# Kernel tuning notes

Measured on AMD Instinct MI355X. Metric: run time of the kernel, lower is better.

Reference implementation:

```python
import jax, jax.numpy as jnp
import numpy as np

B, N, C = 16, 1024, 768
H, HD = 9, 64  # num_active_heads, head_dim


def setup_inputs() -> dict:
    key = jax.random.key(0)
    ks = jax.random.split(key, 5)
    x = jax.random.normal(ks[0], (B, N, C), dtype=jnp.float32)
    qkv_w = jax.random.normal(ks[1], (3 * H * HD, C), dtype=jnp.float32) * (1.0 / np.sqrt(C))
    qkv_b = jax.random.normal(ks[2], (3 * H * HD,), dtype=jnp.float32) * 0.02
    proj_w = jax.random.normal(ks[3], (C, H * HD), dtype=jnp.float32) * (1.0 / np.sqrt(H * HD))
    proj_b = jax.random.normal(ks[4], (C,), dtype=jnp.float32) * 0.02
    return {"x": x, "qkv_w": qkv_w, "qkv_b": qkv_b, "proj_w": proj_w, "proj_b": proj_b}


def reference(x, qkv_w, qkv_b, proj_w, proj_b):
    b, n, c = x.shape
    # qkv projection: [B,N,3*H*HD] -> [3,B,H,N,HD]
    qkv = (x @ qkv_w.T + qkv_b).reshape(b, n, 3, H, HD).transpose(2, 0, 3, 1, 4)
    q, k, v = qkv[0], qkv[1], qkv[2]
    scale = HD ** -0.5
    attn = jnp.einsum('bhqd,bhkd->bhqk', q, k) * scale  # [B,H,N,N]
    attn = jax.nn.softmax(attn, axis=-1)
    out = jnp.einsum('bhqk,bhkd->bhqd', attn, v)  # [B,H,N,HD]
    out = out.transpose(0, 2, 1, 3).reshape(b, n, H * HD)
    return out @ proj_w.T + proj_b
```

## Files before the change

kernel.cpp:

```cpp
#include <hip/hip_runtime.h>


typedef _Float16 f16x8 __attribute__((ext_vector_type(8)));
typedef _Float16 f16x4 __attribute__((ext_vector_type(4)));
typedef __fp16   h16x2 __attribute__((ext_vector_type(2)));
typedef float    f32x4 __attribute__((ext_vector_type(4)));

#define MFMA16(a, b, c) __builtin_amdgcn_mfma_f32_16x16x32_f16(a, b, c, 0, 0, 0)

__device__ __forceinline__ void gld16(const _Float16* g, _Float16* l) {
  __builtin_amdgcn_global_load_lds((const __attribute__((address_space(1))) void*)g,
                                   (__attribute__((address_space(3))) void*)l, 16, 0, 0);
}

__global__ __launch_bounds__(256) void cvt_swz(const float* __restrict__ src,
                                               _Float16* __restrict__ dst,
                                               int rows_src, int cpr, int total) {
  const int g = blockIdx.x * 256 + threadIdx.x;
  if (g >= total) return;
  const int row = g / cpr;
  const int c = g - row * cpr;
  const int L = cpr * 8;
  const int pos = (c & ~7) | ((c ^ row) & 7);
  union { f16x8 v; h16x2 h[4]; } u;
  if (row < rows_src) {
    const float4 a = *(const float4*)(src + row * L + c * 8);
    const float4 b = *(const float4*)(src + row * L + c * 8 + 4);
    u.h[0] = __builtin_amdgcn_cvt_pkrtz(a.x, a.y);
    u.h[1] = __builtin_amdgcn_cvt_pkrtz(a.z, a.w);
    u.h[2] = __builtin_amdgcn_cvt_pkrtz(b.x, b.y);
    u.h[3] = __builtin_amdgcn_cvt_pkrtz(b.z, b.w);
  } else {
    u.v = (f16x8){};
  }
  *(f16x8*)(dst + row * L + pos * 8) = u.v;
}

__global__ __launch_bounds__(256, 4) void gemm1_qkv(const _Float16* __restrict__ A,
                                                    const _Float16* __restrict__ Bw,
                                                    const float* __restrict__ bias,
                                                    _Float16* __restrict__ Qo,
                                                    _Float16* __restrict__ Ko,
                                                    _Float16* __restrict__ Vt) {
  __shared__ __align__(16) _Float16 As[128 * 64];
  __shared__ __align__(16) _Float16 Bs[128 * 64];
  const int tid = threadIdx.x;
  const int wave = tid >> 6, lane = tid & 63;
  const int lo = lane & 15, hi = lane >> 4;
  const int wm = (wave >> 1) * 64, wn = (wave & 1) * 64;
  const int g = blockIdx.x;
  const int xcd = g & 7, i = g >> 3;
  const int mg = i / 56, l56 = i - mg * 56;
  const int mtl = l56 / 14, ntl = l56 - mtl * 14;
  const int mt = mg * 4 + mtl;
  const int m0 = (xcd * 16 + mt) * 128, n0 = ntl * 128;
  f32x4 acc[4][4] = {};
  for (int k0 = 0; k0 < 768; k0 += 64) {
    __syncthreads();
    #pragma unroll
    for (int j = 0; j < 4; ++j) {
      const int seg = wave * 4 + j;
      const int gr = seg * 8 + (lane >> 3), gc = (lane & 7) << 3;
      gld16(A + (m0 + gr) * 768 + k0 + gc, As + seg * 512);
      gld16(Bw + (n0 + gr) * 768 + k0 + gc, Bs + seg * 512);
    }
    __syncthreads();
    #pragma unroll
    for (int ks = 0; ks < 2; ++ks) {
      f16x8 af[4], bf[4];
      const int p = ((ks * 4 + hi) ^ (lo & 7)) << 3;
      #pragma unroll
      for (int t = 0; t < 4; ++t) {
        af[t] = *(const f16x8*)(As + (wm + t * 16 + lo) * 64 + p);
        bf[t] = *(const f16x8*)(Bs + (wn + t * 16 + lo) * 64 + p);
      }
      #pragma unroll
      for (int mt2 = 0; mt2 < 4; ++mt2)
        #pragma unroll
        for (int nt = 0; nt < 4; ++nt)
          acc[mt2][nt] = MFMA16(af[mt2], bf[nt], acc[mt2][nt]);
    }
  }
  const int b = m0 >> 10;
  const int nrbase = (m0 & 1023) + wm;
  #pragma unroll
  for (int nt = 0; nt < 4; ++nt) {
    const int n = n0 + wn + nt * 16 + lo;
    if (n < 1728) {
      const float bv = bias[n];
      const int t3 = n / 576;
      const int rem = n - t3 * 576;
      const int hh = rem >> 6, d = rem & 63;
      const int bh16 = (b * 9 + hh) << 16;
      if (t3 == 2) {
        _Float16* dv = Vt + bh16 + d * 1024;
        #pragma unroll
        for (int mt2 = 0; mt2 < 4; ++mt2) {
          const int nr = nrbase + mt2 * 16 + hi * 4;
          const int c = nr >> 3;
          const int pos = (c & ~7) | ((c ^ d) & 7);
          union { f16x4 v; h16x2 h[2]; } u;
          u.h[0] = __builtin_amdgcn_cvt_pkrtz(acc[mt2][nt][0] + bv, acc[mt2][nt][1] + bv);
          u.h[1] = __builtin_amdgcn_cvt_pkrtz(acc[mt2][nt][2] + bv, acc[mt2][nt][3] + bv);
          *(f16x4*)(dv + pos * 8 + (nr & 7)) = u.v;
        }
      } else if (t3 == 1) {
        _Float16* dk = Ko + bh16;
        const int ch = d >> 3, dl = d & 7;
        #pragma unroll
        for (int mt2 = 0; mt2 < 4; ++mt2) {
          const int nr = nrbase + mt2 * 16 + hi * 4;
          #pragma unroll
          for (int i2 = 0; i2 < 4; ++i2) {
            const int t = nr + i2;
            dk[t * 64 + ((ch ^ (t & 7)) << 3) + dl] = (_Float16)(acc[mt2][nt][i2] + bv);
          }
        }
      } else {
        _Float16* dq = Qo + bh16 + d;
        #pragma unroll
        for (int mt2 = 0; mt2 < 4; ++mt2) {
          const int nr = nrbase + mt2 * 16 + hi * 4;
          #pragma unroll
          for (int i2 = 0; i2 < 4; ++i2)
            dq[(nr + i2) * 64] = (_Float16)(acc[mt2][nt][i2] + bv);
        }
      }
    }
  }
}

__global__ __launch_bounds__(256, 3) void attn_fused(const _Float16* __restrict__ Qg,
                                                     const _Float16* __restrict__ Kg,
                                                     const _Float16* __restrict__ Vtg,
                                                     _Float16* __restrict__ Og) {
  __shared__ __align__(16) _Float16 Ks[2][64 * 64];
  __shared__ __align__(16) _Float16 Vts[2][64 * 64];
  __shared__ __align__(16) _Float16 Ps[4][16 * 64];
  const int tid = threadIdx.x;
  const int wave = tid >> 6, lane = tid & 63;
  const int lo = lane & 15, hi = lane >> 4;
  const int bid = blockIdx.x;
  const int xcd = bid & 7, idx = bid >> 3;
  const int bh = xcd * 18 + (idx >> 3);
  const int q0 = (idx & 7) << 7;
  const _Float16* Qp  = Qg + (bh << 16);
  const _Float16* Kp  = Kg + (bh << 16);
  const _Float16* Vtp = Vtg + (bh << 16);

  #define ISSUE(T0, NB) do {                                                        \
    _Pragma("unroll")                                                               \
    for (int j = 0; j < 2; ++j) {                                                   \
      const int seg = wave * 2 + j;                                                 \
      gld16(Kp + ((T0) + seg * 8 + (lane >> 3)) * 64 + ((lane & 7) << 3),           \
            &Ks[NB][seg * 512]);                                                    \
      gld16(Vtp + (seg * 8 + (lane >> 3)) * 1024 + (T0) + ((lane & 7) << 3),        \
            &Vts[NB][seg * 512]);                                                   \
    }                                                                               \
  } while (0)

  ISSUE(0, 0);

  f16x8 qf0[2], qf1[2];
  const _Float16* qrow0 = Qp + (q0 + wave * 16 + lo) * 64;
  const _Float16* qrow1 = qrow0 + 64 * 64;
  qf0[0] = *(const f16x8*)(qrow0 + hi * 8);
  qf0[1] = *(const f16x8*)(qrow0 + (4 + hi) * 8);
  qf1[0] = *(const f16x8*)(qrow1 + hi * 8);
  qf1[1] = *(const f16x8*)(qrow1 + (4 + hi) * 8);

  float m0_ = -1e30f, l0_ = 0.f, m1_ = -1e30f, l1_ = 0.f;
  f32x4 accO0[4] = {}, accO1[4] = {};
  const float cs = 0.125f * 1.44269504f;
  _Float16* Pw = Ps[wave];

  #define GRP(S, AO, MR, LR) do {                                                   \
    float rmax = -1e30f;                                                            \
    _Pragma("unroll")                                                               \
    for (int tt = 0; tt < 4; ++tt)                                                  \
      rmax = fmaxf(rmax, fmaxf(fmaxf(S[tt][0], S[tt][1]), fmaxf(S[tt][2], S[tt][3])));\
    rmax = fmaxf(rmax, __shfl_xor(rmax, 16, 64));                                   \
    rmax = fmaxf(rmax, __shfl_xor(rmax, 32, 64));                                   \
    const float mnew = fmaxf(MR, rmax * cs);                                        \
    const float alpha = __builtin_amdgcn_exp2f(MR - mnew);                          \
    float rsum = 0.f;                                                               \
    _Pragma("unroll")                                                               \
    for (int tt = 0; tt < 4; ++tt) {                                                \
      const float p0 = __builtin_amdgcn_exp2f(fmaf(S[tt][0], cs, -mnew));           \
      const float p1 = __builtin_amdgcn_exp2f(fmaf(S[tt][1], cs, -mnew));           \
      const float p2 = __builtin_amdgcn_exp2f(fmaf(S[tt][2], cs, -mnew));           \
      const float p3 = __builtin_amdgcn_exp2f(fmaf(S[tt][3], cs, -mnew));           \
      rsum += (p0 + p1) + (p2 + p3);                                                \
      union { f16x4 v; h16x2 h[2]; } u;                                             \
      u.h[0] = __builtin_amdgcn_cvt_pkrtz(p0, p1);                                  \
      u.h[1] = __builtin_amdgcn_cvt_pkrtz(p2, p3);                                  \
      const int c = 2 * tt + (hi >> 1);                                             \
      *(f16x4*)(Pw + lo * 64 + (((c ^ lo) & 7) << 3) + ((hi & 1) << 2)) = u.v;      \
    }                                                                               \
    rsum += __shfl_xor(rsum, 16, 64);                                               \
    rsum += __shfl_xor(rsum, 32, 64);                                               \
    LR = LR * alpha + rsum;                                                         \
    MR = mnew;                                                                      \
    _Pragma("unroll")                                                               \
    for (int dt = 0; dt < 4; ++dt) AO[dt] *= alpha;                                 \
    _Pragma("unroll")                                                               \
    for (int ks2 = 0; ks2 < 2; ++ks2) {                                             \
      const int c = 4 * ks2 + hi;                                                   \
      const f16x8 pf = *(const f16x8*)(Pw + lo * 64 + (((c ^ lo) & 7) << 3));       \
      _Pragma("unroll")                                                             \
      for (int dt = 0; dt < 4; ++dt) {                                              \
        const int dd = dt * 16 + lo;                                                \
        const f16x8 vf = *(const f16x8*)(Vc + dd * 64 + (((c ^ dd) & 7) << 3));     \
        AO[dt] = MFMA16(vf, pf, AO[dt]);                                            \
      }                                                                             \
    }                                                                               \
  } while (0)

  #define COMPUTE(CB) do {                                                          \
    const _Float16* Kc = Ks[CB];                                                    \
    const _Float16* Vc = Vts[CB];                                                   \
    f32x4 s0_[4] = {}, s1_[4] = {};                                                 \
    _Pragma("unroll")                                                               \
    for (int tt = 0; tt < 4; ++tt)                                                  \
      _Pragma("unroll")                                                             \
      for (int ks = 0; ks < 2; ++ks) {                                              \
        const f16x8 kf = *(const f16x8*)(Kc + (tt * 16 + lo) * 64 +                 \
                                         (((ks * 4 + hi) ^ (lo & 7)) << 3));        \
        s0_[tt] = MFMA16(kf, qf0[ks], s0_[tt]);                                     \
        s1_[tt] = MFMA16(kf, qf1[ks], s1_[tt]);                                     \
      }                                                                             \
    GRP(s0_, accO0, m0_, l0_);                                                      \
    GRP(s1_, accO1, m1_, l1_);                                                      \
  } while (0)

  #define STEP_PRE(TN0, CB) do {                                                    \
    ISSUE(TN0, (CB) ^ 1);                                                           \
    asm volatile("s_waitcnt vmcnt(4)" ::: "memory");            \
    __builtin_amdgcn_sched_barrier(0);                                              \
    __builtin_amdgcn_s_barrier();         \
    COMPUTE(CB);                                                                    \
    __builtin_amdgcn_sched_barrier(0);                                              \
    __builtin_amdgcn_s_barrier();           \
  } while (0)

  #define STEP_LAST(CB) do {                                                        \
    asm volatile("s_waitcnt vmcnt(0)" ::: "memory");               \
    __builtin_amdgcn_sched_barrier(0);                                              \
    __builtin_amdgcn_s_barrier();                                                   \
    COMPUTE(CB);                                                                    \
  } while (0)

  #pragma unroll 1
  for (int it = 0; it < 7; ++it) {
    STEP_PRE((2 * it + 1) << 6, 0);
    STEP_PRE((2 * it + 2) << 6, 1);
  }
  STEP_PRE(15 << 6, 0);
  STEP_LAST(1);

  const int b = bh / 9, hh = bh - b * 9;
  {
    const float inv = 1.f / l0_;
    const int rq = (b << 10) + q0 + wave * 16 + lo;
    #pragma unroll
    for (int dt = 0; dt < 4; ++dt) {
      union { f16x4 v; h16x2 h[2]; } u;
      u.h[0] = __builtin_amdgcn_cvt_pkrtz(accO0[dt][0] * inv, accO0[dt][1] * inv);
      u.h[1] = __builtin_amdgcn_cvt_pkrtz(accO0[dt][2] * inv, accO0[dt][3] * inv);
      const int c = hh * 8 + dt * 2 + (hi >> 1);
      const int pos = (c & ~7) | ((c ^ rq) & 7);
      *(f16x4*)(Og + rq * 576 + pos * 8 + ((hi & 1) << 2)) = u.v;
    }
  }
  {
    const float inv = 1.f / l1_;
    const int rq = (b << 10) + q0 + 64 + wave * 16 + lo;
    #pragma unroll
    for (int dt = 0; dt < 4; ++dt) {
      union { f16x4 v; h16x2 h[2]; } u;
      u.h[0] = __builtin_amdgcn_cvt_pkrtz(accO1[dt][0] * inv, accO1[dt][1] * inv);
      u.h[1] = __builtin_amdgcn_cvt_pkrtz(accO1[dt][2] * inv, accO1[dt][3] * inv);
      const int c = hh * 8 + dt * 2 + (hi >> 1);
      const int pos = (c & ~7) | ((c ^ rq) & 7);
      *(f16x4*)(Og + rq * 576 + pos * 8 + ((hi & 1) << 2)) = u.v;
    }
  }
  #undef STEP_LAST
  #undef STEP_PRE
  #undef COMPUTE
  #undef GRP
  #undef ISSUE
}

__global__ __launch_bounds__(256, 4) void gemm3_proj(const _Float16* __restrict__ A,
                                                     const _Float16* __restrict__ Bw,
                                                     const float* __restrict__ bias,
                                                     float* __restrict__ out) {
  __shared__ __align__(16) _Float16 As[128 * 64];
  __shared__ __align__(16) _Float16 Bs[128 * 64];
  const int tid = threadIdx.x;
  const int wave = tid >> 6, lane = tid & 63;
  const int lo = lane & 15, hi = lane >> 4;
  const int wm = (wave >> 1) * 64, wn = (wave & 1) * 64;
  const int g = blockIdx.x;
  const int xcd = g & 7, i = g >> 3;
  const int mt = i / 6, ntl = i - mt * 6;
  const int m0 = (xcd * 16 + mt) * 128, n0 = ntl * 128;
  f32x4 acc[4][4] = {};
  for (int k0 = 0; k0 < 576; k0 += 64) {
    __syncthreads();
    #pragma unroll
    for (int j = 0; j < 4; ++j) {
      const int seg = wave * 4 + j;
      const int gr = seg * 8 + (lane >> 3), gc = (lane & 7) << 3;
      gld16(A + (m0 + gr) * 576 + k0 + gc, As + seg * 512);
      gld16(Bw + (n0 + gr) * 576 + k0 + gc, Bs + seg * 512);
    }
    __syncthreads();
    #pragma unroll
    for (int ks = 0; ks < 2; ++ks) {
      f16x8 af[4], bf[4];
      const int p = ((ks * 4 + hi) ^ (lo & 7)) << 3;
      #pragma unroll
      for (int t = 0; t < 4; ++t) {
        af[t] = *(const f16x8*)(As + (wm + t * 16 + lo) * 64 + p);
        bf[t] = *(const f16x8*)(Bs + (wn + t * 16 + lo) * 64 + p);
      }
      #pragma unroll
      for (int mt2 = 0; mt2 < 4; ++mt2)
        #pragma unroll
        for (int nt = 0; nt < 4; ++nt)
          acc[mt2][nt] = MFMA16(af[mt2], bf[nt], acc[mt2][nt]);
    }
  }
  #pragma unroll
  for (int nt = 0; nt < 4; ++nt) {
    const int n = n0 + wn + nt * 16 + lo;
    const float bv = bias[n];
    #pragma unroll
    for (int mt2 = 0; mt2 < 4; ++mt2) {
      const int mrow = m0 + wm + mt2 * 16 + hi * 4;
      #pragma unroll
      for (int i2 = 0; i2 < 4; ++i2)
        out[(mrow + i2) * 768 + n] = acc[mt2][nt][i2] + bv;
    }
  }
}

extern "C" void kernel_launch(void* const* d_in, const int* in_sizes, int n_in,
                              void* d_out, int out_size, void* d_ws, size_t ws_size,
                              hipStream_t stream) {
  const float* x      = (const float*)d_in[0];
  const float* qkv_w  = (const float*)d_in[1];
  const float* qkv_b  = (const float*)d_in[2];
  const float* proj_w = (const float*)d_in[3];
  const float* proj_b = (const float*)d_in[4];
  float* out = (float*)d_out;

  char* ws = (char*)d_ws;
  _Float16* x16 = (_Float16*)(ws + 0);
  _Float16* w1p = (_Float16*)(ws + 25165824);
  _Float16* w2h = (_Float16*)(ws + 27918336);
  _Float16* Qh  = (_Float16*)(ws + 28803072);
  _Float16* Kh  = (_Float16*)(ws + 47677440);
  _Float16* Vth = (_Float16*)(ws + 66551808);
  _Float16* Oh  = (_Float16*)(ws + 85426176);

  cvt_swz<<<6144, 256, 0, stream>>>(x, x16, 16384, 96, 16384 * 96);
  cvt_swz<<<672, 256, 0, stream>>>(qkv_w, w1p, 1728, 96, 1792 * 96);
  cvt_swz<<<216, 256, 0, stream>>>(proj_w, w2h, 768, 72, 768 * 72);
  gemm1_qkv<<<1792, 256, 0, stream>>>(x16, w1p, qkv_b, Qh, Kh, Vth);
  attn_fused<<<1152, 256, 0, stream>>>(Qh, Kh, Vth, Oh);
  gemm3_proj<<<768, 256, 0, stream>>>(Oh, w2h, proj_b, out);
}
```

Baseline: 268.2 us.

## Restructure attention loop: single barrier per step, lazy rescale, shared V fragments

The attention kernel now computes on the current K/V buffer while the next tile's loads are in flight, then waits and barriers once per step instead of twice. The softmax skips the max update and accumulator rescale when the new row maximum stays within a threshold of the running one. V fragments are loaded once and reused for both query halves, with separate P buffers per half. The QKV GEMM tile mapping is also simplified, dropping the grouped M ordering, which may reduce L2 locality.

```diff
diff --git a/kernel.cpp b/kernel.cpp
--- a/kernel.cpp
+++ b/kernel.cpp
@@ -50,9 +50,7 @@
   const int wm = (wave >> 1) * 64, wn = (wave & 1) * 64;
   const int g = blockIdx.x;
   const int xcd = g & 7, i = g >> 3;
-  const int mg = i / 56, l56 = i - mg * 56;
-  const int mtl = l56 / 14, ntl = l56 - mtl * 14;
-  const int mt = mg * 4 + mtl;
+  const int mt = i / 14, ntl = i - mt * 14;
   const int m0 = (xcd * 16 + mt) * 128, n0 = ntl * 128;
   f32x4 acc[4][4] = {};
   for (int k0 = 0; k0 < 768; k0 += 64) {
@@ -136,7 +134,7 @@
                                                      _Float16* __restrict__ Og) {
   __shared__ __align__(16) _Float16 Ks[2][64 * 64];
   __shared__ __align__(16) _Float16 Vts[2][64 * 64];
-  __shared__ __align__(16) _Float16 Ps[4][16 * 64];
+  __shared__ __align__(16) _Float16 Ps[8][16 * 64];
   const int tid = threadIdx.x;
   const int wave = tid >> 6, lane = tid & 63;
   const int lo = lane & 15, hi = lane >> 4;
@@ -161,134 +159,148 @@
 
   ISSUE(0, 0);
 
-  f16x8 qf0[2], qf1[2];
   const _Float16* qrow0 = Qp + (q0 + wave * 16 + lo) * 64;
   const _Float16* qrow1 = qrow0 + 64 * 64;
-  qf0[0] = *(const f16x8*)(qrow0 + hi * 8);
-  qf0[1] = *(const f16x8*)(qrow0 + (4 + hi) * 8);
-  qf1[0] = *(const f16x8*)(qrow1 + hi * 8);
-  qf1[1] = *(const f16x8*)(qrow1 + (4 + hi) * 8);
-
-  float m0_ = -1e30f, l0_ = 0.f, m1_ = -1e30f, l1_ = 0.f;
-  f32x4 accO0[4] = {}, accO1[4] = {};
+  const f16x8 qf0a = *(const f16x8*)(qrow0 + hi * 8);
+  const f16x8 qf0b = *(const f16x8*)(qrow0 + (4 + hi) * 8);
+  const f16x8 qf1a = *(const f16x8*)(qrow1 + hi * 8);
+  const f16x8 qf1b = *(const f16x8*)(qrow1 + (4 + hi) * 8);
+
+  float mA = -1e30f, lA = 0.f, mB = -1e30f, lB = 0.f;
+  f32x4 oA0 = {}, oA1 = {}, oA2 = {}, oA3 = {};
+  f32x4 oB0 = {}, oB1 = {}, oB2 = {}, oB3 = {};
   const float cs = 0.125f * 1.44269504f;
-  _Float16* Pw = Ps[wave];
-
-  #define GRP(S, AO, MR, LR) do {                                                   \
-    float rmax = -1e30f;                                                            \
-    _Pragma("unroll")                                                               \
-    for (int tt = 0; tt < 4; ++tt)                                                  \
-      rmax = fmaxf(rmax, fmaxf(fmaxf(S[tt][0], S[tt][1]), fmaxf(S[tt][2], S[tt][3])));\
+  _Float16* PwA = Ps[wave];
+  _Float16* PwB = Ps[wave + 4];
+
+  asm volatile("s_waitcnt vmcnt(0)" ::: "memory");
+  __builtin_amdgcn_sched_barrier(0);
+  __builtin_amdgcn_s_barrier();
+
+  #define STT(TT) do {                                                              \
+    const f16x8 kfa = *(const f16x8*)(Kc + ((TT) * 16 + lo) * 64 +                  \
+                                      ((hi ^ (lo & 7)) << 3));                      \
+    sA##TT = MFMA16(kfa, qf0a, sA##TT);                                             \
+    sB##TT = MFMA16(kfa, qf1a, sB##TT);                                             \
+    const f16x8 kfb = *(const f16x8*)(Kc + ((TT) * 16 + lo) * 64 +                  \
+                                      (((4 + hi) ^ (lo & 7)) << 3));                \
+    sA##TT = MFMA16(kfb, qf0b, sA##TT);                                             \
+    sB##TT = MFMA16(kfb, qf1b, sB##TT);                                             \
+  } while (0)
+
+  #define SMTT(S, TT, PW, MNEW, RSUM) do {                                          \
+    const float p0 = __builtin_amdgcn_exp2f(fmaf(S[0], cs, -(MNEW)));               \
+    const float p1 = __builtin_amdgcn_exp2f(fmaf(S[1], cs, -(MNEW)));               \
+    const float p2 = __builtin_amdgcn_exp2f(fmaf(S[2], cs, -(MNEW)));               \
+    const float p3 = __builtin_amdgcn_exp2f(fmaf(S[3], cs, -(MNEW)));               \
+    RSUM += (p0 + p1) + (p2 + p3);                                                  \
+    union { f16x4 v; h16x2 h[2]; } u;                                               \
+    u.h[0] = __builtin_amdgcn_cvt_pkrtz(p0, p1);                                    \
+    u.h[1] = __builtin_amdgcn_cvt_pkrtz(p2, p3);                                    \
+    const int c = 2 * (TT) + (hi >> 1);                                             \
+    *(f16x4*)((PW) + lo * 64 + (((c ^ lo) & 7) << 3) + ((hi & 1) << 2)) = u.v;      \
+  } while (0)
+
+  #define GRPSM(S0, S1, S2, S3, MR, LR, AO0, AO1, AO2, AO3, PW) do {                \
+    float rmax = fmaxf(fmaxf(fmaxf(S0[0], S0[1]), fmaxf(S0[2], S0[3])),             \
+                 fmaxf(fmaxf(fmaxf(S1[0], S1[1]), fmaxf(S1[2], S1[3])),             \
+                 fmaxf(fmaxf(fmaxf(S2[0], S2[1]), fmaxf(S2[2], S2[3])),             \
+                       fmaxf(fmaxf(S3[0], S3[1]), fmaxf(S3[2], S3[3])))));          \
     rmax = fmaxf(rmax, __shfl_xor(rmax, 16, 64));                                   \
     rmax = fmaxf(rmax, __shfl_xor(rmax, 32, 64));                                   \
-    const float mnew = fmaxf(MR, rmax * cs);                                        \
-    const float alpha = __builtin_amdgcn_exp2f(MR - mnew);                          \
+    const float rs_ = rmax * cs;                                                    \
+    const bool nsk = !__all(rs_ <= (MR) + 8.f);                                     \
+    const float mnew = nsk ? fmaxf(MR, rs_) : (MR);                                 \
+    const float alpha = nsk ? __builtin_amdgcn_exp2f((MR) - mnew) : 1.f;            \
     float rsum = 0.f;                                                               \
-    _Pragma("unroll")                                                               \
-    for (int tt = 0; tt < 4; ++tt) {                                                \
-      const float p0 = __builtin_amdgcn_exp2f(fmaf(S[tt][0], cs, -mnew));           \
-      const float p1 = __builtin_amdgcn_exp2f(fmaf(S[tt][1], cs, -mnew));           \
-      const float p2 = __builtin_amdgcn_exp2f(fmaf(S[tt][2], cs, -mnew));           \
-      const float p3 = __builtin_amdgcn_exp2f(fmaf(S[tt][3], cs, -mnew));           \
-      rsum += (p0 + p1) + (p2 + p3);                                                \
-      union { f16x4 v; h16x2 h[2]; } u;                                             \
-      u.h[0] = __builtin_amdgcn_cvt_pkrtz(p0, p1);                                  \
-      u.h[1] = __builtin_amdgcn_cvt_pkrtz(p2, p3);                                  \
-      const int c = 2 * tt + (hi >> 1);                                             \
-      *(f16x4*)(Pw + lo * 64 + (((c ^ lo) & 7) << 3) + ((hi & 1) << 2)) = u.v;      \
-    }                                                                               \
+    SMTT(S0, 0, PW, mnew, rsum);                                                    \
+    SMTT(S1, 1, PW, mnew, rsum);                                                    \
+    SMTT(S2, 2, PW, mnew, rsum);                                                    \
+    SMTT(S3, 3, PW, mnew, rsum);                                                    \
     rsum += __shfl_xor(rsum, 16, 64);                                               \
     rsum += __shfl_xor(rsum, 32, 64);                                               \
     LR = LR * alpha + rsum;                                                         \
     MR = mnew;                                                                      \
-    _Pragma("unroll")                                                               \
-    for (int dt = 0; dt < 4; ++dt) AO[dt] *= alpha;                                 \
-    _Pragma("unroll")                                                               \
-    for (int ks2 = 0; ks2 < 2; ++ks2) {                                             \
-      const int c = 4 * ks2 + hi;                                                   \
-      const f16x8 pf = *(const f16x8*)(Pw + lo * 64 + (((c ^ lo) & 7) << 3));       \
-      _Pragma("unroll")                                                             \
-      for (int dt = 0; dt < 4; ++dt) {                                              \
-        const int dd = dt * 16 + lo;                                                \
-        const f16x8 vf = *(const f16x8*)(Vc + dd * 64 + (((c ^ dd) & 7) << 3));     \
-        AO[dt] = MFMA16(vf, pf, AO[dt]);                                            \
-      }                                                                             \
-    }                                                                               \
+    if (nsk) { AO0 *= alpha; AO1 *= alpha; AO2 *= alpha; AO3 *= alpha; }            \
+  } while (0)
+
+  #define PVKS(KS2) do {                                                            \
+    const int c2 = 4 * (KS2) + hi;                                                  \
+    const int po = ((c2 ^ lo) & 7) << 3;                                            \
+    const f16x8 pfA = *(const f16x8*)(PwA + lo * 64 + po);                          \
+    const f16x8 pfB = *(const f16x8*)(PwB + lo * 64 + po);                          \
+    const f16x8 vf0 = *(const f16x8*)(Vc + (lo) * 64 + po);                         \
+    oA0 = MFMA16(vf0, pfA, oA0); oB0 = MFMA16(vf0, pfB, oB0);                       \
+    const f16x8 vf1 = *(const f16x8*)(Vc + (16 + lo) * 64 + po);                    \
+    oA1 = MFMA16(vf1, pfA, oA1); oB1 = MFMA16(vf1, pfB, oB1);                       \
+    const f16x8 vf2 = *(const f16x8*)(Vc + (32 + lo) * 64 + po);                    \
+    oA2 = MFMA16(vf2, pfA, oA2); oB2 = MFMA16(vf2, pfB, oB2);                       \
+    const f16x8 vf3 = *(const f16x8*)(Vc + (48 + lo) * 64 + po);                    \
+    oA3 = MFMA16(vf3, pfA, oA3); oB3 = MFMA16(vf3, pfB, oB3);                       \
   } while (0)
 
   #define COMPUTE(CB) do {                                                          \
     const _Float16* Kc = Ks[CB];                                                    \
     const _Float16* Vc = Vts[CB];                                                   \
-    f32x4 s0_[4] = {}, s1_[4] = {};                                                 \
-    _Pragma("unroll")                                                               \
-    for (int tt = 0; tt < 4; ++tt)                                                  \
-      _Pragma("unroll")                                                             \
-      for (int ks = 0; ks < 2; ++ks) {                                              \
-        const f16x8 kf = *(const f16x8*)(Kc + (tt * 16 + lo) * 64 +                 \
-                                         (((ks * 4 + hi) ^ (lo & 7)) << 3));        \
-        s0_[tt] = MFMA16(kf, qf0[ks], s0_[tt]);                                     \
-        s1_[tt] = MFMA16(kf, qf1[ks], s1_[tt]);                                     \
-      }                                                                             \
-    GRP(s0_, accO0, m0_, l0_);                                                      \
-    GRP(s1_, accO1, m1_, l1_);                                                      \
-  } while (0)
-
-  #define STEP_PRE(TN0, CB) do {                                                    \
+    f32x4 sA0 = {}, sA1 = {}, sA2 = {}, sA3 = {};                                   \
+    f32x4 sB0 = {}, sB1 = {}, sB2 = {}, sB3 = {};                                   \
+    STT(0); STT(1); STT(2); STT(3);                                                 \
+    GRPSM(sA0, sA1, sA2, sA3, mA, lA, oA0, oA1, oA2, oA3, PwA);                     \
+    GRPSM(sB0, sB1, sB2, sB3, mB, lB, oB0, oB1, oB2, oB3, PwB);                     \
+    PVKS(0);                                                                        \
+    PVKS(1);                                                                        \
+  } while (0)
+
+  #define STEPSB(TN0, CB) do {                                                      \
     ISSUE(TN0, (CB) ^ 1);                                                           \
-    asm volatile("s_waitcnt vmcnt(4)" ::: "memory");            \
+    COMPUTE(CB);                                                                    \
+    asm volatile("s_waitcnt vmcnt(0)" ::: "memory");       \
     __builtin_amdgcn_sched_barrier(0);                                              \
     __builtin_amdgcn_s_barrier();         \
-    COMPUTE(CB);                                                                    \
-    __builtin_amdgcn_sched_barrier(0);                                              \
-    __builtin_amdgcn_s_barrier();           \
-  } while (0)
-
-  #define STEP_LAST(CB) do {                                                        \
-    asm volatile("s_waitcnt vmcnt(0)" ::: "memory");               \
-    __builtin_amdgcn_sched_barrier(0);                                              \
-    __builtin_amdgcn_s_barrier();                                                   \
-    COMPUTE(CB);                                                                    \
   } while (0)
 
   #pragma unroll 1
   for (int it = 0; it < 7; ++it) {
-    STEP_PRE((2 * it + 1) << 6, 0);
-    STEP_PRE((2 * it + 2) << 6, 1);
-  }
-  STEP_PRE(15 << 6, 0);
-  STEP_LAST(1);
+    STEPSB((2 * it + 1) << 6, 0);
+    STEPSB((2 * it + 2) << 6, 1);
+  }
+  STEPSB(15 << 6, 0);
+  COMPUTE(1);
 
   const int b = bh / 9, hh = bh - b * 9;
-  {
-    const float inv = 1.f / l0_;
-    const int rq = (b << 10) + q0 + wave * 16 + lo;
-    #pragma unroll
-    for (int dt = 0; dt < 4; ++dt) {
-      union { f16x4 v; h16x2 h[2]; } u;
-      u.h[0] = __builtin_amdgcn_cvt_pkrtz(accO0[dt][0] * inv, accO0[dt][1] * inv);
-      u.h[1] = __builtin_amdgcn_cvt_pkrtz(accO0[dt][2] * inv, accO0[dt][3] * inv);
-      const int c = hh * 8 + dt * 2 + (hi >> 1);
-      const int pos = (c & ~7) | ((c ^ rq) & 7);
-      *(f16x4*)(Og + rq * 576 + pos * 8 + ((hi & 1) << 2)) = u.v;
-    }
-  }
-  {
-    const float inv = 1.f / l1_;
-    const int rq = (b << 10) + q0 + 64 + wave * 16 + lo;
-    #pragma unroll
-    for (int dt = 0; dt < 4; ++dt) {
-      union { f16x4 v; h16x2 h[2]; } u;
-      u.h[0] = __builtin_amdgcn_cvt_pkrtz(accO1[dt][0] * inv, accO1[dt][1] * inv);
-      u.h[1] = __builtin_amdgcn_cvt_pkrtz(accO1[dt][2] * inv, accO1[dt][3] * inv);
-      const int c = hh * 8 + dt * 2 + (hi >> 1);
-      const int pos = (c & ~7) | ((c ^ rq) & 7);
-      *(f16x4*)(Og + rq * 576 + pos * 8 + ((hi & 1) << 2)) = u.v;
-    }
-  }
-  #undef STEP_LAST
-  #undef STEP_PRE
+  #define OWRITE(AO0, AO1, AO2, AO3, LR, QOFF) do {                                 \
+    const float inv = 1.f / (LR);                                                   \
+    const int rq = (b << 10) + q0 + (QOFF) + wave * 16 + lo;                        \
+    union { f16x4 v; h16x2 h[2]; } u;                                               \
+    int c, pos;                                                                     \
+    u.h[0] = __builtin_amdgcn_cvt_pkrtz(AO0[0] * inv, AO0[1] * inv);                \
+    u.h[1] = __builtin_amdgcn_cvt_pkrtz(AO0[2] * inv, AO0[3] * inv);                \
+    c = hh * 8 + 0 * 2 + (hi >> 1); pos = (c & ~7) | ((c ^ rq) & 7);                \
+    *(f16x4*)(Og + rq * 576 + pos * 8 + ((hi & 1) << 2)) = u.v;                     \
+    u.h[0] = __builtin_amdgcn_cvt_pkrtz(AO1[0] * inv, AO1[1] * inv);                \
+    u.h[1] = __builtin_amdgcn_cvt_pkrtz(AO1[2] * inv, AO1[3] * inv);                \
+    c = hh * 8 + 1 * 2 + (hi >> 1); pos = (c & ~7) | ((c ^ rq) & 7);                \
+    *(f16x4*)(Og + rq * 576 + pos * 8 + ((hi & 1) << 2)) = u.v;                     \
+    u.h[0] = __builtin_amdgcn_cvt_pkrtz(AO2[0] * inv, AO2[1] * inv);                \
+    u.h[1] = __builtin_amdgcn_cvt_pkrtz(AO2[2] * inv, AO2[3] * inv);                \
+    c = hh * 8 + 2 * 2 + (hi >> 1); pos = (c & ~7) | ((c ^ rq) & 7);                \
+    *(f16x4*)(Og + rq * 576 + pos * 8 + ((hi & 1) << 2)) = u.v;                     \
+    u.h[0] = __builtin_amdgcn_cvt_pkrtz(AO3[0] * inv, AO3[1] * inv);                \
+    u.h[1] = __builtin_amdgcn_cvt_pkrtz(AO3[2] * inv, AO3[3] * inv);                \
+    c = hh * 8 + 3 * 2 + (hi >> 1); pos = (c & ~7) | ((c ^ rq) & 7);                \
+    *(f16x4*)(Og + rq * 576 + pos * 8 + ((hi & 1) << 2)) = u.v;                     \
+  } while (0)
+
+  OWRITE(oA0, oA1, oA2, oA3, lA, 0);
+  OWRITE(oB0, oB1, oB2, oB3, lB, 64);
+
+  #undef OWRITE
+  #undef STEPSB
   #undef COMPUTE
-  #undef GRP
+  #undef PVKS
+  #undef GRPSM
+  #undef SMTT
+  #undef STT
   #undef ISSUE
 }
 
```

After: 258.0 us. -3.8%, faster.
